# Kernel tuning notes

Measured on AMD Instinct MI355X. Metric: run time of the kernel, lower is better.

## Reference

```python
import jax, jax.numpy as jnp
import numpy as np

STRIDE = 16
SIZES = np.array([128.0, 256.0, 512.0], np.float32)
RATIOS = np.array([0.5, 1.0, 2.0], np.float32)
N_POS, N_NEG = 32, 32          # n_sample=64, pos_ratio=0.5
POS_THR, NEG_THR = 0.7, 0.2
W_CONF, W_REG = 1.0, 5.0


def _conv(x, w, b, stride, pad):
    y = jax.lax.conv_general_dilated(x, w, (stride, stride), [(pad, pad), (pad, pad)],
                                     dimension_numbers=('NCHW', 'OIHW', 'NCHW'))
    return y + b[None, :, None, None]


def _anchors(fw, fh, stride):
    # 9 anchors per center: 3 sizes x 3 aspect ratios
    ws = (SIZES[:, None] * np.sqrt(RATIOS)[None, :]).reshape(-1)
    hs = (SIZES[:, None] / np.sqrt(RATIOS)[None, :]).reshape(-1)
    wh = jnp.asarray(np.stack([ws, hs], -1))                      # (9,2)
    cx = (jnp.arange(fw, dtype=jnp.float32) + 0.5) * stride
    cy = (jnp.arange(fh, dtype=jnp.float32) + 0.5) * stride
    gx, gy = jnp.meshgrid(cx, cy, indexing='ij')                  # x-major, like the torch list comp
    ctr = jnp.stack([gx, gy], -1)[:, :, None, :]                  # (fw,fh,1,2)
    tl = ctr - wh / 2.0
    xywh = jnp.concatenate([tl, jnp.broadcast_to(wh, tl.shape)], -1)  # (fw,fh,9,4)
    return xywh.reshape(-1, 4)


def _xywh_to_xyxy(b):
    return jnp.concatenate([b[:, :2], b[:, :2] + b[:, 2:]], -1)


def _iou(a, b):  # a [N,4], b [M,4], xyxy
    lt = jnp.maximum(a[:, None, :2], b[None, :, :2])
    rb = jnp.minimum(a[:, None, 2:], b[None, :, 2:])
    inter = jnp.clip(rb - lt, 0.0).prod(-1)
    aa = (a[:, 2] - a[:, 0]) * (a[:, 3] - a[:, 1])
    ab = (b[:, 2] - b[:, 0]) * (b[:, 3] - b[:, 1])
    return inter / (aa[:, None] + ab[None, :] - inter)


def _head_flat(y, per):  # [1, 9*per, H, W] -> [W*H*9, per], matching anchor flatten order
    _, _, H, W = y.shape
    return y[0].reshape(9, per, H, W).transpose(3, 2, 0, 1).reshape(-1, per)


def _apply_offsets(boxes, off):  # decode proposals from xyxy boxes + (dx,dy,dw,dh)
    w = boxes[:, 2] - boxes[:, 0]; h = boxes[:, 3] - boxes[:, 1]
    cx = boxes[:, 0] + 0.5 * w;    cy = boxes[:, 1] + 0.5 * h
    ncx = cx + off[:, 0] * w;      ncy = cy + off[:, 1] * h
    nw = w * jnp.exp(off[:, 2]);   nh = h * jnp.exp(off[:, 3])
    return jnp.stack([ncx - nw / 2, ncy - nh / 2, ncx + nw / 2, ncy + nh / 2], -1)


def _box_offset(anc, gt):
    aw = anc[:, 2] - anc[:, 0]; ah = anc[:, 3] - anc[:, 1]
    acx = anc[:, 0] + 0.5 * aw; acy = anc[:, 1] + 0.5 * ah
    gw = gt[:, 2] - gt[:, 0];   gh = gt[:, 3] - gt[:, 1]
    gcx = gt[:, 0] + 0.5 * gw;  gcy = gt[:, 1] + 0.5 * gh
    return jnp.stack([(gcx - acx) / aw, (gcy - acy) / ah,
                      jnp.log(gw / aw), jnp.log(gh / ah)], -1)


def setup_inputs():
    key = jax.random.key(0)
    ks = jax.random.split(key, 12)
    img_data = jax.random.normal(ks[0], (1, 3, 1600, 1600), jnp.float32)
    x1 = jax.random.uniform(ks[1], (64,), minval=0.0, maxval=1400.0)
    y1 = jax.random.uniform(ks[2], (64,), minval=0.0, maxval=1400.0)
    bw = jax.random.uniform(ks[3], (64,), minval=32.0, maxval=200.0)
    bh = jax.random.uniform(ks[4], (64,), minval=32.0, maxval=200.0)
    gt_boxes = jnp.stack([x1, y1, x1 + bw, y1 + bh], -1)[None]   # [1,64,4], all valid (no -1 pad)
    gt_classes = jax.random.randint(ks[5], (1, 64), 1, 21, jnp.int32)
    def w(k, shape, fan):
        return jax.random.normal(k, shape, jnp.float32) * np.float32(np.sqrt(2.0 / fan))
    return dict(
        img_data=img_data, gt_boxes=gt_boxes, gt_classes=gt_classes,
        w1=w(ks[6], (64, 3, 7, 7), 3 * 49),      b1=jnp.zeros(64, jnp.float32),
        w2=w(ks[7], (256, 64, 3, 3), 64 * 9),    b2=jnp.zeros(256, jnp.float32),
        w_rpn=w(ks[8], (256, 256, 3, 3), 256 * 9), b_rpn=jnp.zeros(256, jnp.float32),
        w_cls=w(ks[9], (18, 256, 1, 1), 256),    b_cls=jnp.zeros(18, jnp.float32),
        w_reg=w(ks[10], (36, 256, 1, 1), 256),   b_reg=jnp.zeros(36, jnp.float32),
    )


def reference(img_data, gt_boxes, gt_classes, w1, b1, w2, b2, w_rpn, b_rpn, w_cls, b_cls, w_reg, b_reg):
    # --- feature extractor (total stride 16) ---
    fm = jax.nn.relu(_conv(img_data, w1, b1, 4, 3))
    fm = jax.nn.relu(_conv(fm, w2, b2, 4, 1))            # [1,256,100,100]
    H, W = fm.shape[2], fm.shape[3]
    # --- anchors + IoU matching ---
    anchors_xywh = _anchors(W, H, STRIDE)                # [N,4] xywh
    anchors_xyxy = _xywh_to_xyxy(anchors_xywh)
    gt = gt_boxes[0]                                     # [M,4], all valid
    ious = _iou(anchors_xyxy, gt)                        # [N,M]
    N = ious.shape[0]
    gt_max = ious.max(0)                                 # best iou per gt
    is_gt_best = (ious == gt_max[None, :]).any(1)        # torch: where(iou == gt_max)[0]
    anc_argmax = ious.argmax(1)
    anc_max = ious.max(1)
    labels = jnp.full((N,), -1.0, jnp.float32)
    labels = jnp.where(anc_max < NEG_THR, 0.0, labels)
    labels = jnp.where(is_gt_best, 1.0, labels)
    labels = jnp.where(anc_max > POS_THR, 1.0, labels)
    # --- deterministic pos/neg sampling (fixed sizes; replaces randperm subsampling) ---
    idx = jnp.arange(N, dtype=jnp.float32)
    _, pos_index = jax.lax.top_k(jnp.where(labels == 1.0, anc_max, -1.0), N_POS)
    _, neg_index = jax.lax.top_k(jnp.where(labels == 0.0, 1e6 - idx, -1e9), N_NEG)
    bboxes_pos = anchors_xyxy[pos_index]                 # box_convert(xywh->xyxy) of pos anchors
    # --- proposal module (RPN head) ---
    h = jax.nn.relu(_conv(fm, w_rpn, b_rpn, 1, 1))
    cls = _head_flat(_conv(h, w_cls, b_cls, 1, 0), 2)    # [N,2]
    reg = _head_flat(_conv(h, w_reg, b_reg, 1, 0), 4)    # [N,4]
    pos_score = cls[pos_index]
    neg_score = cls[neg_index]
    offset_pos = reg[pos_index]
    proposals = _apply_offsets(bboxes_pos, offset_pos)
    # --- losses ---
    gt_offset = _box_offset(bboxes_pos, gt[anc_argmax[pos_index]])
    logits = jnp.concatenate([pos_score, neg_score], 0)  # [64,2]
    tgt = jnp.concatenate([jnp.ones(N_POS, jnp.int32), jnp.zeros(N_NEG, jnp.int32)])
    logp = jax.nn.log_softmax(logits, -1)
    cls_loss = -logp[jnp.arange(N_POS + N_NEG), tgt].mean()
    d = gt_offset - offset_pos
    ad = jnp.abs(d)
    reg_loss = jnp.where(ad < 1.0, 0.5 * d * d, ad - 0.5).mean()
    total_rpn_loss = W_CONF * cls_loss + W_REG * reg_loss
    gt_cls_pos = gt_classes[0][anc_argmax[pos_index]]
    return (total_rpn_loss, fm, proposals, pos_index, gt_cls_pos)
```

## Files before the change

### kernel.cpp

```cpp
#include <hip/hip_runtime.h>
#include <math.h>


#define CAP 4096

typedef __attribute__((ext_vector_type(8))) short bf16x8;
typedef __attribute__((ext_vector_type(4))) float f32x4;

__device__ __forceinline__ void dma16(const void* g, void* l) {
    __builtin_amdgcn_global_load_lds((const __attribute__((address_space(1))) void*)g,
                                     (__attribute__((address_space(3))) void*)l, 16, 0, 0);
}

#define OFF_F1T     0
#define OFF_FMT     5171328
#define OFF_CPART   6503040
#define OFF_RPART   7223040
#define OFF_WA1     8663040
#define OFF_W9_2    8672448
#define OFF_W9_3    8746176
#define OFF_WTC     9041088
#define OFF_WTG     9045696
#define OFF_AARG    9054912
#define OFF_NEGM    9144912
#define OFF_POSM    9147728
#define OFF_GTMAX   9150544
#define OFF_CANDS   9150688
#define OFF_CANDI   9154784
#define OFF_IMGB    9158880

__device__ __forceinline__ unsigned short f2bf(float f) {
    unsigned int u = __float_as_uint(f);
    u += 0x7fffu + ((u >> 16) & 1u);
    return (unsigned short)(u >> 16);
}

__device__ __forceinline__ void anchor_box(int i, float& x0, float& y0,
                                           float& x1, float& y1, float& area) {
#pragma clang fp contract(off)
    const float sizes[3]  = {128.f, 256.f, 512.f};
    const float ratios[3] = {0.5f, 1.f, 2.f};
    int a = i % 9;
    int q = i / 9;
    int iy = q % 100;
    int ix = q / 100;
    int s = a / 3, r = a % 3;
    float sq = sqrtf(ratios[r]);
    float w = sizes[s] * sq;
    float h = sizes[s] / sq;
    float cx = ((float)ix + 0.5f) * 16.0f;
    float cy = ((float)iy + 0.5f) * 16.0f;
    x0 = cx - w * 0.5f;
    y0 = cy - h * 0.5f;
    x1 = x0 + w;
    y1 = y0 + h;
    area = (x1 - x0) * (y1 - y0);
}

__device__ __forceinline__ float iou_one(float ax0, float ay0, float ax1, float ay1, float aa,
                                         float bx0, float by0, float bx1, float by1, float ab) {
#pragma clang fp contract(off)
    float ltx = fmaxf(ax0, bx0), lty = fmaxf(ay0, by0);
    float rbx = fminf(ax1, bx1), rby = fminf(ay1, by1);
    float iw = fmaxf(rbx - ltx, 0.0f);
    float ih = fmaxf(rby - lty, 0.0f);
    float inter = iw * ih;
    return inter / ((aa + ab) - inter);
}

__global__ __launch_bounds__(256) void setup_kernel(const float* __restrict__ wc, float* __restrict__ wtc,
                                                    const float* __restrict__ wg, float* __restrict__ wtg,
                                                    const float* __restrict__ w1, unsigned short* __restrict__ wa1,
                                                    const float* __restrict__ w2, unsigned short* __restrict__ w9_2,
                                                    const float* __restrict__ wr, unsigned short* __restrict__ w9_3,
                                                    unsigned int* __restrict__ f1t_u, unsigned int* __restrict__ fmt_u,
                                                    unsigned int* __restrict__ gtmax,
                                                    const float* __restrict__ img, unsigned short* __restrict__ imgb) {
    int i = blockIdx.x * 256 + threadIdx.x;
    if (i < 65) { gtmax[i] = 0u; return; }
    i -= 65;
    if (i < 103040) {
        if (i < 51328) {
            int p = i >> 5, part = i & 31;
            int x, y;
            if (p < 804) { y = (p < 402) ? 0 : 401; x = p % 402; }
            else { int j = p - 804; x = (j < 400) ? 0 : 401; y = 1 + (j % 400); }
            f1t_u[(y * 402 + x) * 32 + part] = 0u;
        } else {
            int i2 = i - 51328;
            int p = i2 >> 7, part = i2 & 127;
            int x, y;
            if (p < 204) { y = (p < 102) ? 0 : 101; x = p % 102; }
            else { int j = p - 204; x = (j < 100) ? 0 : 101; y = 1 + (j % 100); }
            fmt_u[(y * 102 + x) * 128 + part] = 0u;
        }
        return;
    }
    i -= 103040;
    if (i < 4608) { int c = i / 256, k = i - c * 256; wtc[k * 18 + c] = wc[i]; return; }
    i -= 4608;
    if (i < 9216) { int c = i / 256, k = i - c * 256; wtg[k * 36 + c] = wg[i]; return; }
    i -= 9216;
    if (i < 12288) {
        int oc = i / 192, k = i - oc * 192;
        int q = k >> 3, kx = k & 7;
        int ky = q / 3, ic = q - (q / 3) * 3;
        wa1[i] = (q < 21 && kx < 7) ? f2bf(w1[oc * 147 + ic * 49 + ky * 7 + kx])
                                    : (unsigned short)0;
        return;
    }
    i -= 12288;
    if (i < 147456) {
        int cc = i >> 14;
        int rem = i & 16383;
        int ocT = rem >> 10;
        int rem2 = rem & 1023;
        int kcl = rem2 >> 9;
        int lane = (rem2 & 511) >> 3;
        int e = rem2 & 7;
        int oc = ocT * 16 + (lane & 15);
        int ic = kcl * 32 + (lane >> 4) * 8 + e;
        w9_2[i] = f2bf(w2[(oc * 64 + ic) * 9 + cc]);
        return;
    }
    i -= 147456;
    if (i < 589824) {
        int cc = i >> 14;
        int rem = i & 16383;
        int ocT = rem >> 10;
        int rem2 = rem & 1023;
        int kcl = rem2 >> 9;
        int lane = (rem2 & 511) >> 3;
        int e = rem2 & 7;
        int kk = cc >> 2, chv = cc & 3;
        int oc = ocT * 16 + (lane & 15);
        int icl = kcl * 32 + (lane >> 4) * 8 + e;
        w9_3[i] = f2bf(wr[(oc * 256 + chv * 64 + icl) * 9 + kk]);
        return;
    }
    i -= 589824;
    if (i < 7680000) {
        int ic = i / 2560000;
        int rem = i - ic * 2560000;
        int y = rem / 1600, x = rem - (rem / 1600) * 1600;
        imgb[((size_t)(ic * 1608 + y + 3)) * 1608 + x + 3] = f2bf(img[((size_t)(ic * 1600 + y)) * 1600 + x]);
        return;
    }
    i -= 7680000;
    if (i < 38592) {
        int ic = i / 12864;
        int rem = i - ic * 12864;
        int r8 = rem / 1608, xp = rem - r8 * 1608;
        int yp = (r8 < 3) ? r8 : (1600 + r8);
        imgb[((size_t)(ic * 1608 + yp)) * 1608 + xp] = 0;
        return;
    }
    i -= 38592;
    if (i < 28800) {
        int ic = i / 9600;
        int rem = i - ic * 9600;
        int y = rem / 6, xi = rem - (rem / 6) * 6;
        int xp = (xi < 3) ? xi : (1602 + xi);
        imgb[((size_t)(ic * 1608 + y + 3)) * 1608 + xp] = 0;
    }
}

__device__ __forceinline__ void iou1_body(int bid, int t, const float* __restrict__ gt,
                                          int* __restrict__ aarg, unsigned int* __restrict__ gtmax) {
    __shared__ float sg1[64][4];
    __shared__ float sarea1[64];
    __shared__ unsigned int smax1[64];
    if (t < 64) {
#pragma clang fp contract(off)
        float b0 = gt[t * 4 + 0], b1 = gt[t * 4 + 1];
        float b2 = gt[t * 4 + 2], b3 = gt[t * 4 + 3];
        sg1[t][0] = b0; sg1[t][1] = b1; sg1[t][2] = b2; sg1[t][3] = b3;
        sarea1[t] = (b2 - b0) * (b3 - b1);
        smax1[t] = 0u;
    }
    __syncthreads();
    int i = bid * 256 + t;
    int iq = min(i, 89999);
    float x0, y0, x1, y1, aa;
    anchor_box(iq, x0, y0, x1, y1, aa);
    float best = -1.f;
    int bestj = 0;
    for (int j = 0; j < 64; j++) {
        float v = iou_one(x0, y0, x1, y1, aa, sg1[j][0], sg1[j][1], sg1[j][2], sg1[j][3], sarea1[j]);
        if (v > best) { best = v; bestj = j; }
        float vm = v;
#pragma unroll
        for (int off = 32; off > 0; off >>= 1) vm = fmaxf(vm, __shfl_xor(vm, off));
        if ((t & 63) == 0) atomicMax(&smax1[j], __float_as_uint(vm));
    }
    if (i < 90000) aarg[i] = bestj;
    __syncthreads();
    if (t < 64) atomicMax(&gtmax[t], smax1[t]);
}

__device__ __forceinline__ void iou2_body(int bid, int t, const float* __restrict__ gt,
                                          const unsigned int* __restrict__ gtmax,
                                          unsigned long long* __restrict__ negmask,
                                          unsigned long long* __restrict__ posmask,
                                          float* __restrict__ cand_s, int* __restrict__ cand_i,
                                          unsigned int* __restrict__ cnt) {
    __shared__ float sg2[64][4];
    __shared__ float sarea2[64];
    __shared__ float sgm2[64];
    if (t < 64) {
#pragma clang fp contract(off)
        float b0 = gt[t * 4 + 0], b1 = gt[t * 4 + 1];
        float b2 = gt[t * 4 + 2], b3 = gt[t * 4 + 3];
        sg2[t][0] = b0; sg2[t][1] = b1; sg2[t][2] = b2; sg2[t][3] = b3;
        sarea2[t] = (b2 - b0) * (b3 - b1);
        sgm2[t] = __uint_as_float(gtmax[t]);
    }
    __syncthreads();
    int i = bid * 512 + t;
    if (i >= 90000) return;
    float x0, y0, x1, y1, aa;
    anchor_box(i, x0, y0, x1, y1, aa);
    float best = -1.f;
    bool isbest = false;
    for (int j = 0; j < 64; j++) {
        float v = iou_one(x0, y0, x1, y1, aa, sg2[j][0], sg2[j][1], sg2[j][2], sg2[j][3], sarea2[j]);
        if (v > best) best = v;
        if (v == sgm2[j]) isbest = true;
    }
    float label = -1.f;
    if (best < 0.2f) label = 0.f;
    if (isbest) label = 1.f;
    if (best > 0.7f) label = 1.f;
    unsigned long long negb = __ballot(label == 0.f);
    unsigned long long posb = __ballot(label == 1.f);
    if ((t & 63) == 0) { negmask[i >> 6] = negb; posmask[i >> 6] = posb; }
    if (label == 1.f) {
        unsigned int p = atomicAdd(cnt, 1u);
        if (p < CAP) { cand_s[p] = best; cand_i[p] = i; }
    }
}

__device__ __forceinline__ void conv1_body(int bx, int oy, int t,
                                           const unsigned short* __restrict__ imgb,
                                           const unsigned short* __restrict__ wA,
                                           const float* __restrict__ bias,
                                           unsigned short* __restrict__ f1t) {
    __shared__ __align__(16) unsigned char smem[13312];
    unsigned short* win = (unsigned short*)smem;
    unsigned short* tileT = (unsigned short*)smem;
    int wave = t >> 6, lane = t & 63;
    int quad = lane >> 4, l16 = lane & 15;
    int ox0 = bx * 64;
    int col0 = ox0 * 4;
    int gy0 = 4 * oy - 3;
    const size_t ZROW = ((size_t)(2 * 1608 + 1606)) * 1608;

    for (int o = wave; o < 13; o += 4) {
        int q = o * 64 + lane;
        int r = q / 33;
        int c = q - r * 33;
        int rc = min(r, 20);
        int ky = rc / 3, ic = rc - (rc / 3) * 3;
        int yp = gy0 + ky + 3;
        size_t offm = ((size_t)(ic * 1608 + yp)) * 1608 + col0 + c * 8;
        size_t offz = ZROW + (size_t)(q - 693) * 8;
        dma16(imgb + ((r < 21) ? offm : offz), (char*)smem + o * 1024);
    }
    bf16x8 afr[6];
    {
        const bf16x8* ap = (const bf16x8*)(wA + (wave * 16 + l16) * 192 + quad * 8);
#pragma unroll
        for (int c = 0; c < 6; c++) afr[c] = ap[c * 4];
    }
    __syncthreads();

    f32x4 acc[4];
#pragma unroll
    for (int j = 0; j < 4; j++) acc[j] = (f32x4){0.f, 0.f, 0.f, 0.f};
#pragma unroll
    for (int ch = 0; ch < 6; ch++) {
        const unsigned short* wrow = win + (ch * 4 + quad) * 264;
#pragma unroll
        for (int j = 0; j < 4; j++) {
            int px = j * 16 + l16;
            const unsigned long long* bp = (const unsigned long long*)(wrow + 4 * px);
            union { unsigned long long u[2]; bf16x8 v; } uu;
            uu.u[0] = bp[0];
            uu.u[1] = bp[1];
            acc[j] = __builtin_amdgcn_mfma_f32_16x16x32_bf16(afr[ch], uu.v, acc[j], 0, 0, 0);
        }
    }
    __syncthreads();
#pragma unroll
    for (int reg = 0; reg < 4; reg++) {
        int oc = wave * 16 + quad * 4 + reg;
        float bv = bias[oc];
#pragma unroll
        for (int j = 0; j < 4; j++) {
            int px = j * 16 + l16;
            tileT[px * 72 + oc] = f2bf(fmaxf(acc[j][reg] + bv, 0.f));
        }
    }
    __syncthreads();
    int px = t >> 2, part = t & 3;
    int ox = ox0 + px;
    if (ox < 400) {
        int row = (oy + 1) * 402 + ox + 1;
        uint4 v0 = *(const uint4*)(tileT + px * 72 + part * 16);
        uint4 v1 = *(const uint4*)(tileT + px * 72 + part * 16 + 8);
        *(uint4*)(f1t + row * 64 + part * 16) = v0;
        *(uint4*)(f1t + row * 64 + part * 16 + 8) = v1;
    }
}

__global__ __launch_bounds__(256, 4) void conv1_iou1(const unsigned short* __restrict__ imgb,
                                                     const unsigned short* __restrict__ wA,
                                                     const float* __restrict__ bias,
                                                     unsigned short* __restrict__ f1t,
                                                     const float* __restrict__ gt,
                                                     int* __restrict__ aarg,
                                                     unsigned int* __restrict__ gtmax) {
    int t = threadIdx.x;
    if (blockIdx.x < 7) {
        conv1_body(blockIdx.x, blockIdx.y, t, imgb, wA, bias, f1t);
    } else {
        int bid = blockIdx.y;
        if (bid < 352) iou1_body(bid, t, gt, aarg, gtmax);
    }
}

template<int ICC, int RS, int S, bool WRT, bool HEAD>
__device__ __forceinline__ void conv_body(int xs, int y, int t,
                                          const unsigned short* __restrict__ Bt,
                                          const unsigned short* __restrict__ A9,
                                          const float* __restrict__ bias,
                                          float* __restrict__ outF,
                                          unsigned short* __restrict__ outT,
                                          const float* __restrict__ wtc,
                                          const float* __restrict__ wtg,
                                          float* __restrict__ cpart,
                                          float* __restrict__ rpart) {
    constexpr int NC = ICC / 64;
    constexpr int PXB = 13;
    constexpr int HC = S * (PXB - 1) + 3;
    constexpr int CHW = ICC / 8;
    constexpr int TOT = 3 * HC * CHW;
    constexpr int OPS = (TOT + 63) / 64;
    constexpr int BB = OPS * 1024;
    constexpr int SMB = HEAD ? (16384 + 256 * 14 * 4) : BB;
    __shared__ __align__(16) unsigned char smem[SMB < BB ? BB : SMB];
    unsigned short* blds = (unsigned short*)smem;
    float* sred = (float*)smem;
    float* hlds = (float*)(smem + 16384);

    int wave = t >> 6, lane = t & 63;
    int PX = min(PXB, 100 - xs * PXB);

    for (int o = wave; o < OPS; o += 8) {
        int q = min(o * 64 + lane, TOT - 1);
        int row = q / CHW;
        int e = q - row * CHW;
        int ky = row / HC;
        int c = row - ky * HC;
        int s = (S == 4) ? (e ^ ((c >> 2) & 7)) : (e ^ (row & 7));
        const unsigned short* src = Bt + ((size_t)(S * y + ky) * RS + S * xs * PXB + c) * ICC + s * 8;
        dma16(src, (char*)smem + o * 1024);
    }

    int ow = wave & 3, kg = wave >> 2;
    int quad = lane >> 4, l16 = lane & 15;
    int oc0 = ow * 64;
    int pxe = min(l16, PX - 1);
    int swp = pxe & 7;

    f32x4 acc[4];
#pragma unroll
    for (int mt = 0; mt < 4; mt++) acc[mt] = (f32x4){0.f, 0.f, 0.f, 0.f};

    const bf16x8* Av = (const bf16x8*)A9;
    __syncthreads();

    constexpr int NS = (NC == 1) ? 9 : 36;
    bf16x8 afA[4], afB[4];
    {
        int cc0 = (NC == 1) ? 0 : kg * 18;
        int kl0 = (NC == 1) ? kg : 0;
#pragma unroll
        for (int mt = 0; mt < 4; mt++)
            afA[mt] = Av[(size_t)cc0 * 2048 + (ow * 4 + mt) * 128 + kl0 * 64 + lane];
    }
    auto kstep = [&](int s, bf16x8 (&cur)[4], bf16x8 (&nxt)[4]) {
        int cc  = (NC == 1) ? s : kg * 18 + (s >> 1);
        int kcl = (NC == 1) ? kg : (s & 1);
        int pass = cc / NC, ch = cc - pass * NC;
        int ky = pass / 3, kx = pass - (pass / 3) * 3;
        int row = ky * HC + S * pxe + kx;
        int ck = kcl * 4 + quad;
        int chunk = (S == 4) ? (ck ^ swp) : ((ch * 8 + ck) ^ (row & 7));
        bf16x8 bf = *(const bf16x8*)(blds + row * ICC + chunk * 8);
        if (s + 1 < NS) {
            int cn = (NC == 1) ? (s + 1) : kg * 18 + ((s + 1) >> 1);
            int kn = (NC == 1) ? kg : ((s + 1) & 1);
#pragma unroll
            for (int mt = 0; mt < 4; mt++)
                nxt[mt] = Av[(size_t)cn * 2048 + (ow * 4 + mt) * 128 + kn * 64 + lane];
        }
#pragma unroll
        for (int mt = 0; mt < 4; mt++)
            acc[mt] = __builtin_amdgcn_mfma_f32_16x16x32_bf16(cur[mt], bf, acc[mt], 0, 0, 0);
    };
#pragma unroll
    for (int s2 = 0; s2 < NS; s2 += 2) {
        kstep(s2, afA, afB);
        if (s2 + 1 < NS) kstep(s2 + 1, afB, afA);
    }

    __syncthreads();
    if (kg == 1) {
#pragma unroll
        for (int mt = 0; mt < 4; mt++)
            *(f32x4*)(sred + ((ow * 4 + mt) * 64 + lane) * 4) = acc[mt];
    }
    __syncthreads();
    if (kg == 0) {
#pragma unroll
        for (int mt = 0; mt < 4; mt++) {
            f32x4 o = *(const f32x4*)(sred + ((ow * 4 + mt) * 64 + lane) * 4);
            acc[mt] = acc[mt] + o;
        }
#pragma unroll
        for (int mt = 0; mt < 4; mt++) {
#pragma unroll
            for (int reg = 0; reg < 4; reg++) {
                int oc = oc0 + mt * 16 + quad * 4 + reg;
                float bv = bias[oc];
                int pl = l16;
                if (pl < PX) {
                    float v = fmaxf(acc[mt][reg] + bv, 0.f);
                    if (HEAD) {
                        hlds[oc * 14 + pl] = v;
                    } else {
                        int p = y * 100 + xs * PXB + pl;
                        outF[oc * 10000 + p] = v;
                        if (WRT) {
                            int r = (y + 1) * 102 + xs * PXB + pl + 1;
                            outT[r * 256 + oc] = f2bf(v);
                        }
                    }
                }
            }
        }
    }
    if (HEAD) {
        __syncthreads();
        int base = y * 100 + xs * PXB;
        for (int it = t; it < 2808; it += 512) {
            int ch = it / 702;
            int r = it - ch * 702;
            int j = r / 13;
            int p = r - j * 13;
            if (p < PX) {
                int jc = (j < 18) ? j : (j - 18);
                const float* wt = (j < 18) ? (wtc + jc) : (wtg + jc);
                int stride = (j < 18) ? 18 : 36;
                int ic0 = ch * 64;
                float acc2 = 0.f;
#pragma unroll 8
                for (int ic = 0; ic < 64; ic++)
                    acc2 += hlds[(ic0 + ic) * 14 + p] * wt[(ic0 + ic) * stride];
                float* dst = (j < 18) ? (cpart + (ch * 18 + jc) * 10000)
                                      : (rpart + (ch * 36 + jc) * 10000);
                dst[base + p] = acc2;
            }
        }
    }
}

__global__ __launch_bounds__(512, 4) void conv2_iou2(const unsigned short* __restrict__ Bt,
                                                     const unsigned short* __restrict__ A9,
                                                     const float* __restrict__ bias,
                                                     float* __restrict__ outF,
                                                     unsigned short* __restrict__ outT,
                                                     const float* __restrict__ gt,
                                                     const unsigned int* __restrict__ gtmax,
                                                     unsigned long long* __restrict__ negmask,
                                                     unsigned long long* __restrict__ posmask,
                                                     float* __restrict__ cand_s,
                                                     int* __restrict__ cand_i,
                                                     unsigned int* __restrict__ cnt) {
    int t = threadIdx.x;
    if (blockIdx.x < 8) {
        conv_body<64, 402, 4, true, false>(blockIdx.x, blockIdx.y, t, Bt, A9, bias,
                                           outF, outT, nullptr, nullptr, nullptr, nullptr);
    } else {
        int bid = (blockIdx.x - 8) * 100 + blockIdx.y;
        if (bid < 176) iou2_body(bid, t, gt, gtmax, negmask, posmask, cand_s, cand_i, cnt);
    }
}

__global__ __launch_bounds__(512, 4) void conv3_head(const unsigned short* __restrict__ Bt,
                                                     const unsigned short* __restrict__ A9,
                                                     const float* __restrict__ bias,
                                                     const float* __restrict__ wtc,
                                                     const float* __restrict__ wtg,
                                                     float* __restrict__ cpart,
                                                     float* __restrict__ rpart) {
    conv_body<256, 102, 1, false, true>(blockIdx.x, blockIdx.y, threadIdx.x, Bt, A9, bias,
                                        nullptr, nullptr, wtc, wtg, cpart, rpart);
}

__device__ __forceinline__ unsigned long long shflx64(unsigned long long v, int m) {
    int lo = __shfl_xor((int)(unsigned)(v & 0xFFFFFFFFull), m);
    int hi = __shfl_xor((int)(unsigned)(v >> 32), m);
    return ((unsigned long long)(unsigned)hi << 32) | (unsigned)lo;
}

__device__ int wave_first32(const unsigned long long* __restrict__ mask,
                            bool invert, int* __restrict__ outIdx, int lane) {
    const int NW = 1407;
    const int WPT = 22;
    unsigned long long mw[WPT];
    int cnt = 0;
#pragma unroll
    for (int u = 0; u < WPT; u++) {
        int w = lane * WPT + u;
        unsigned long long m = 0ull;
        if (w < NW) {
            m = mask[w];
            if (invert) m = ~m;
            if (w == NW - 1) m &= 0xFFFFull;
        }
        mw[u] = m;
        cnt += __builtin_popcountll(m);
    }
    int inc = cnt;
#pragma unroll
    for (int off = 1; off < 64; off <<= 1) {
        int v = __shfl_up(inc, off);
        if (lane >= off) inc += v;
    }
    int total = __shfl(inc, 63);
    int pref = inc - cnt;
    if (pref < 32) {
#pragma unroll
        for (int u = 0; u < WPT; u++) {
            unsigned long long m = mw[u];
            int wbase = (lane * WPT + u) * 64;
            while (m && pref < 32) {
                int b = __builtin_ctzll(m);
                outIdx[pref++] = wbase + b;
                m &= m - 1;
            }
        }
    }
    return total;
}

__global__ __launch_bounds__(64) void tail_kernel(const unsigned long long* __restrict__ negmask,
                                                  const unsigned long long* __restrict__ posmask,
                                                  const float* __restrict__ cand_s,
                                                  const int* __restrict__ cand_i,
                                                  const unsigned int* __restrict__ cnt,
                                                  const float* __restrict__ cpart,
                                                  const float* __restrict__ rpart,
                                                  const float* __restrict__ bcls,
                                                  const float* __restrict__ breg,
                                                  const int* __restrict__ aarg,
                                                  const float* __restrict__ gt,
                                                  const int* __restrict__ gtc,
                                                  float* __restrict__ out) {
    __shared__ unsigned long long keys[CAP + 32];
    __shared__ int sfill[32];
    __shared__ int spidx[32];
    __shared__ int snidx[32];
    int lane = threadIdx.x;

    int ncand = min((int)*cnt, CAP);
    for (int c = lane; c < ncand; c += 64) {
        unsigned u = __float_as_uint(cand_s[c]);
        u ^= (u & 0x80000000u) ? 0xFFFFFFFFu : 0x80000000u;
        keys[c] = ((unsigned long long)u << 32) | (0xFFFFFFFFu - (unsigned)cand_i[c]);
    }
    int ntot = ncand;
    if (ncand < 32) {
        int tot = wave_first32(posmask, true, sfill, lane);
        int nfill = min(tot, 32);
        unsigned um1 = __float_as_uint(-1.0f) ^ 0xFFFFFFFFu;
        for (int k2 = lane; k2 < nfill; k2 += 64)
            keys[ncand + k2] = ((unsigned long long)um1 << 32) | (0xFFFFFFFFu - (unsigned)sfill[k2]);
        ntot += nfill;
    }

    unsigned long long lk = 0ull; int ls = -1;
    for (int c = lane; c < ntot; c += 64) {
        unsigned long long k = keys[c];
        if (k > lk) { lk = k; ls = c; }
    }
    for (int s = 0; s < 32; s++) {
        unsigned long long mk = lk;
#pragma unroll
        for (int off = 1; off < 64; off <<= 1) {
            unsigned long long o = shflx64(mk, off);
            if (o > mk) mk = o;
        }
        if (lk == mk && mk != 0ull) {
            spidx[s] = (int)(0xFFFFFFFFu - (unsigned)(mk & 0xFFFFFFFFull));
            keys[ls] = 0ull;
            lk = 0ull; ls = -1;
            for (int c = lane; c < ntot; c += 64) {
                unsigned long long k = keys[c];
                if (k > lk) { lk = k; ls = c; }
            }
        }
    }

    int totn = wave_first32(negmask, false, snidx, lane);
    if (lane == 0) {
        int nf = min(totn, 32);
        for (int s = nf; s < 32; s++) snidx[s] = s;
    }

    {
#pragma clang fp contract(off)
        const int PROP_OFF = 1 + 2560000;
        int t = lane;
        int n = (t < 32) ? spidx[t] : snidx[t - 32];
        int a = n % 9;
        int q = n / 9;
        int iy = q % 100;
        int ix = q / 100;
        int p = iy * 100 + ix;

        float l0 = bcls[a * 2 + 0], l1 = bcls[a * 2 + 1];
        for (int c = 0; c < 4; c++) {
            l0 += cpart[(c * 18 + a * 2 + 0) * 10000 + p];
            l1 += cpart[(c * 18 + a * 2 + 1) * 10000 + p];
        }
        float m = fmaxf(l0, l1);
        float lse = m + logf(expf(l0 - m) + expf(l1 - m));
        float logp = ((t < 32) ? l1 : l0) - lse;
        float cls_sum = logp;
#pragma unroll
        for (int off = 32; off > 0; off >>= 1) cls_sum += __shfl_down(cls_sum, off);

        float reg_sum = 0.f;
        if (t < 32) {
            float offv[4];
#pragma unroll
            for (int k = 0; k < 4; k++) {
                float v = breg[a * 4 + k];
                for (int c = 0; c < 4; c++) v += rpart[(c * 36 + a * 4 + k) * 10000 + p];
                offv[k] = v;
            }
            float x0, y0, x1, y1, aa;
            anchor_box(n, x0, y0, x1, y1, aa);
            float w = x1 - x0, h = y1 - y0;
            float cx = x0 + 0.5f * w, cy = y0 + 0.5f * h;
            float ncx = cx + offv[0] * w, ncy = cy + offv[1] * h;
            float nw = w * expf(offv[2]), nh = h * expf(offv[3]);
            out[PROP_OFF + t * 4 + 0] = ncx - nw * 0.5f;
            out[PROP_OFF + t * 4 + 1] = ncy - nh * 0.5f;
            out[PROP_OFF + t * 4 + 2] = ncx + nw * 0.5f;
            out[PROP_OFF + t * 4 + 3] = ncy + nh * 0.5f;

            int j = aarg[n];
            float g0 = gt[j * 4 + 0], g1 = gt[j * 4 + 1];
            float g2 = gt[j * 4 + 2], g3 = gt[j * 4 + 3];
            float gw = g2 - g0, gh = g3 - g1;
            float gcx = g0 + 0.5f * gw, gcy = g1 + 0.5f * gh;
            float tg[4];
            tg[0] = (gcx - cx) / w;
            tg[1] = (gcy - cy) / h;
            tg[2] = logf(gw / w);
            tg[3] = logf(gh / h);
#pragma unroll
            for (int k = 0; k < 4; k++) {
                float d = tg[k] - offv[k];
                float ad = fabsf(d);
                reg_sum += (ad < 1.f) ? 0.5f * d * d : ad - 0.5f;
            }
            out[PROP_OFF + 128 + t] = (float)n;
            out[PROP_OFF + 160 + t] = (float)gtc[j];
        }
#pragma unroll
        for (int off = 32; off > 0; off >>= 1) reg_sum += __shfl_down(reg_sum, off);
        if (t == 0) {
            float cls_loss = -(cls_sum / 64.f);
            float reg_loss = reg_sum / 128.f;
            out[0] = cls_loss + 5.f * reg_loss;
        }
    }
}

extern "C" void kernel_launch(void* const* d_in, const int* in_sizes, int n_in,
                              void* d_out, int out_size, void* d_ws, size_t ws_size,
                              hipStream_t stream) {
    const float* img = (const float*)d_in[0];
    const float* gt  = (const float*)d_in[1];
    const int*   gtc = (const int*)d_in[2];
    const float* w1  = (const float*)d_in[3];
    const float* b1  = (const float*)d_in[4];
    const float* w2  = (const float*)d_in[5];
    const float* b2  = (const float*)d_in[6];
    const float* wr  = (const float*)d_in[7];
    const float* br  = (const float*)d_in[8];
    const float* wc  = (const float*)d_in[9];
    const float* bc  = (const float*)d_in[10];
    const float* wg  = (const float*)d_in[11];
    const float* bg  = (const float*)d_in[12];
    float* out = (float*)d_out;
    float* ws = (float*)d_ws;

    unsigned short* f1t  = (unsigned short*)(ws + OFF_F1T);
    unsigned short* fmt  = (unsigned short*)(ws + OFF_FMT);
    unsigned short* wa1  = (unsigned short*)(ws + OFF_WA1);
    unsigned short* w9_2 = (unsigned short*)(ws + OFF_W9_2);
    unsigned short* w9_3 = (unsigned short*)(ws + OFF_W9_3);
    unsigned short* imgb = (unsigned short*)(ws + OFF_IMGB);
    float* cpart = ws + OFF_CPART;
    float* rpart = ws + OFF_RPART;
    float* wtc   = ws + OFF_WTC;
    float* wtg   = ws + OFF_WTG;
    int*   aarg  = (int*)(ws + OFF_AARG);
    unsigned long long* negm = (unsigned long long*)(ws + OFF_NEGM);
    unsigned long long* posm = (unsigned long long*)(ws + OFF_POSM);
    unsigned int* gtmax = (unsigned int*)(ws + OFF_GTMAX);
    unsigned int* cnt   = gtmax + 64;
    float* cands = ws + OFF_CANDS;
    int*   candi = (int*)(ws + OFF_CANDI);
    float* fm    = out + 1;

    setup_kernel<<<dim3(33649), dim3(256), 0, stream>>>(wc, wtc, wg, wtg, w1, wa1,
                                                        w2, w9_2, wr, w9_3,
                                                        (unsigned int*)f1t, (unsigned int*)fmt, gtmax,
                                                        img, imgb);

    conv1_iou1<<<dim3(8, 400), dim3(256), 0, stream>>>(imgb, wa1, b1, f1t, gt, aarg, gtmax);
    conv2_iou2<<<dim3(10, 100), dim3(512), 0, stream>>>(f1t, w9_2, b2, fm, fmt,
                                                        gt, gtmax, negm, posm, cands, candi, cnt);
    conv3_head<<<dim3(8, 100), dim3(512), 0, stream>>>(fmt, w9_3, br, wtc, wtg, cpart, rpart);
    tail_kernel<<<dim3(1), dim3(64), 0, stream>>>(negm, posm, cands, candi, cnt,
                                                  cpart, rpart, bc, bg, aarg, gt, gtc, out);
}
```

Baseline: 296.5 us.

## Widen conv tiles to 25 pixels and stage weights through double-buffered LDS

Each conv block now covers 25 output pixels per row, with the 8 waves split into two 16-pixel halves instead of two K-groups. That removes the cross-wave reduction through shared memory. Weight tiles are re-laid out per (cc,kcl) unit and streamed into a double-buffered LDS region with async global-to-LDS loads, replacing per-lane global register loads. Grids shrink to 4 column-blocks per row. The trade-offs are a __syncthreads per K-step, larger LDS use, and 7 of 32 pixel lanes per block wasted, while activation halo reloads are amortised over more pixels.

```diff
diff --git a/kernel.cpp b/kernel.cpp
--- a/kernel.cpp
+++ b/kernel.cpp
@@ -111,13 +111,13 @@
     }
     i -= 12288;
     if (i < 147456) {
-        int cc = i >> 14;
-        int rem = i & 16383;
-        int ocT = rem >> 10;
-        int rem2 = rem & 1023;
-        int kcl = rem2 >> 9;
-        int lane = (rem2 & 511) >> 3;
+        int unit = i >> 13;
+        int rem = i & 8191;
+        int ocT = rem >> 9;
+        int rem2 = rem & 511;
+        int lane = rem2 >> 3;
         int e = rem2 & 7;
+        int cc = unit >> 1, kcl = unit & 1;
         int oc = ocT * 16 + (lane & 15);
         int ic = kcl * 32 + (lane >> 4) * 8 + e;
         w9_2[i] = f2bf(w2[(oc * 64 + ic) * 9 + cc]);
@@ -125,13 +125,13 @@
     }
     i -= 147456;
     if (i < 589824) {
-        int cc = i >> 14;
-        int rem = i & 16383;
-        int ocT = rem >> 10;
-        int rem2 = rem & 1023;
-        int kcl = rem2 >> 9;
-        int lane = (rem2 & 511) >> 3;
+        int unit = i >> 13;
+        int rem = i & 8191;
+        int ocT = rem >> 9;
+        int rem2 = rem & 511;
+        int lane = rem2 >> 3;
         int e = rem2 & 7;
+        int cc = unit >> 1, kcl = unit & 1;
         int kk = cc >> 2, chv = cc & 3;
         int oc = ocT * 16 + (lane & 15);
         int icl = kcl * 32 + (lane >> 4) * 8 + e;
@@ -341,111 +341,81 @@
                                           float* __restrict__ cpart,
                                           float* __restrict__ rpart) {
     constexpr int NC = ICC / 64;
-    constexpr int PXB = 13;
-    constexpr int HC = S * (PXB - 1) + 3;
+    constexpr int HC = S * 24 + 3;
     constexpr int CHW = ICC / 8;
     constexpr int TOT = 3 * HC * CHW;
-    constexpr int OPS = (TOT + 63) / 64;
-    constexpr int BB = OPS * 1024;
-    constexpr int SMB = HEAD ? (16384 + 256 * 14 * 4) : BB;
-    __shared__ __align__(16) unsigned char smem[SMB < BB ? BB : SMB];
+    constexpr int BOPS = (TOT + 63) / 64;
+    constexpr int BB = BOPS * 1024;
+    constexpr int NS = (NC == 1) ? 18 : 72;
+    __shared__ __align__(16) unsigned char smem[BB + 32768];
     unsigned short* blds = (unsigned short*)smem;
-    float* sred = (float*)smem;
-    float* hlds = (float*)(smem + 16384);
+    float* hlds = (float*)(smem + BB);
 
     int wave = t >> 6, lane = t & 63;
-    int PX = min(PXB, 100 - xs * PXB);
-
-    for (int o = wave; o < OPS; o += 8) {
+    int ow = wave & 3, ph = wave >> 2;
+    int quad = lane >> 4, l16 = lane & 15;
+    int oc0 = ow * 64;
+    int pl = ph * 16 + l16;
+    int pxe = min(pl, 24);
+    int swp = pxe & 7;
+
+    for (int o = wave; o < BOPS; o += 8) {
         int q = min(o * 64 + lane, TOT - 1);
         int row = q / CHW;
         int e = q - row * CHW;
         int ky = row / HC;
         int c = row - ky * HC;
-        int s = (S == 4) ? (e ^ ((c >> 2) & 7)) : (e ^ (row & 7));
-        const unsigned short* src = Bt + ((size_t)(S * y + ky) * RS + S * xs * PXB + c) * ICC + s * 8;
-        dma16(src, (char*)smem + o * 1024);
-    }
-
-    int ow = wave & 3, kg = wave >> 2;
-    int quad = lane >> 4, l16 = lane & 15;
-    int oc0 = ow * 64;
-    int pxe = min(l16, PX - 1);
-    int swp = pxe & 7;
+        int sz = (S == 4) ? (e ^ ((c >> 2) & 7)) : (e ^ (row & 7));
+        dma16(Bt + ((size_t)(S * y + ky) * RS + S * xs * 25 + c) * ICC + sz * 8,
+              (char*)smem + o * 1024);
+    }
+    for (int o = wave; o < 16; o += 8)
+        dma16(A9 + (size_t)(o * 64 + lane) * 8, (char*)smem + BB + o * 1024);
 
     f32x4 acc[4];
 #pragma unroll
     for (int mt = 0; mt < 4; mt++) acc[mt] = (f32x4){0.f, 0.f, 0.f, 0.f};
-
-    const bf16x8* Av = (const bf16x8*)A9;
     __syncthreads();
 
-    constexpr int NS = (NC == 1) ? 9 : 36;
-    bf16x8 afA[4], afB[4];
-    {
-        int cc0 = (NC == 1) ? 0 : kg * 18;
-        int kl0 = (NC == 1) ? kg : 0;
-#pragma unroll
-        for (int mt = 0; mt < 4; mt++)
-            afA[mt] = Av[(size_t)cc0 * 2048 + (ow * 4 + mt) * 128 + kl0 * 64 + lane];
-    }
-    auto kstep = [&](int s, bf16x8 (&cur)[4], bf16x8 (&nxt)[4]) {
-        int cc  = (NC == 1) ? s : kg * 18 + (s >> 1);
-        int kcl = (NC == 1) ? kg : (s & 1);
+    for (int u = 0; u < NS; u++) {
+        if (u + 1 < NS) {
+            char* dst = (char*)smem + BB + ((u + 1) & 1) * 16384;
+            const unsigned short* src = A9 + (size_t)(u + 1) * 8192;
+            for (int o = wave; o < 16; o += 8)
+                dma16(src + (size_t)(o * 64 + lane) * 8, dst + o * 1024);
+        }
+        const unsigned short* ab = (const unsigned short*)(smem + BB + (u & 1) * 16384);
+        int cc = u >> 1, kcl = u & 1;
         int pass = cc / NC, ch = cc - pass * NC;
         int ky = pass / 3, kx = pass - (pass / 3) * 3;
         int row = ky * HC + S * pxe + kx;
         int ck = kcl * 4 + quad;
         int chunk = (S == 4) ? (ck ^ swp) : ((ch * 8 + ck) ^ (row & 7));
         bf16x8 bf = *(const bf16x8*)(blds + row * ICC + chunk * 8);
-        if (s + 1 < NS) {
-            int cn = (NC == 1) ? (s + 1) : kg * 18 + ((s + 1) >> 1);
-            int kn = (NC == 1) ? kg : ((s + 1) & 1);
-#pragma unroll
-            for (int mt = 0; mt < 4; mt++)
-                nxt[mt] = Av[(size_t)cn * 2048 + (ow * 4 + mt) * 128 + kn * 64 + lane];
-        }
-#pragma unroll
-        for (int mt = 0; mt < 4; mt++)
-            acc[mt] = __builtin_amdgcn_mfma_f32_16x16x32_bf16(cur[mt], bf, acc[mt], 0, 0, 0);
-    };
-#pragma unroll
-    for (int s2 = 0; s2 < NS; s2 += 2) {
-        kstep(s2, afA, afB);
-        if (s2 + 1 < NS) kstep(s2 + 1, afB, afA);
-    }
-
-    __syncthreads();
-    if (kg == 1) {
-#pragma unroll
-        for (int mt = 0; mt < 4; mt++)
-            *(f32x4*)(sred + ((ow * 4 + mt) * 64 + lane) * 4) = acc[mt];
-    }
-    __syncthreads();
-    if (kg == 0) {
 #pragma unroll
         for (int mt = 0; mt < 4; mt++) {
-            f32x4 o = *(const f32x4*)(sred + ((ow * 4 + mt) * 64 + lane) * 4);
-            acc[mt] = acc[mt] + o;
-        }
-#pragma unroll
-        for (int mt = 0; mt < 4; mt++) {
-#pragma unroll
-            for (int reg = 0; reg < 4; reg++) {
-                int oc = oc0 + mt * 16 + quad * 4 + reg;
-                float bv = bias[oc];
-                int pl = l16;
-                if (pl < PX) {
-                    float v = fmaxf(acc[mt][reg] + bv, 0.f);
-                    if (HEAD) {
-                        hlds[oc * 14 + pl] = v;
-                    } else {
-                        int p = y * 100 + xs * PXB + pl;
-                        outF[oc * 10000 + p] = v;
-                        if (WRT) {
-                            int r = (y + 1) * 102 + xs * PXB + pl + 1;
-                            outT[r * 256 + oc] = f2bf(v);
-                        }
+            bf16x8 af = *(const bf16x8*)(ab + ((ow * 4 + mt) * 64 + lane) * 8);
+            acc[mt] = __builtin_amdgcn_mfma_f32_16x16x32_bf16(af, bf, acc[mt], 0, 0, 0);
+        }
+        __syncthreads();
+    }
+
+#pragma unroll
+    for (int mt = 0; mt < 4; mt++) {
+#pragma unroll
+        for (int reg = 0; reg < 4; reg++) {
+            int oc = oc0 + mt * 16 + quad * 4 + reg;
+            float bv = bias[oc];
+            if (pl < 25) {
+                float v = fmaxf(acc[mt][reg] + bv, 0.f);
+                if (HEAD) {
+                    hlds[oc * 26 + pl] = v;
+                } else {
+                    int p = y * 100 + xs * 25 + pl;
+                    outF[oc * 10000 + p] = v;
+                    if (WRT) {
+                        int r = (y + 1) * 102 + xs * 25 + pl + 1;
+                        outT[r * 256 + oc] = f2bf(v);
                     }
                 }
             }
@@ -453,25 +423,23 @@
     }
     if (HEAD) {
         __syncthreads();
-        int base = y * 100 + xs * PXB;
-        for (int it = t; it < 2808; it += 512) {
-            int ch = it / 702;
-            int r = it - ch * 702;
-            int j = r / 13;
-            int p = r - j * 13;
-            if (p < PX) {
-                int jc = (j < 18) ? j : (j - 18);
-                const float* wt = (j < 18) ? (wtc + jc) : (wtg + jc);
-                int stride = (j < 18) ? 18 : 36;
-                int ic0 = ch * 64;
-                float acc2 = 0.f;
+        int base = y * 100 + xs * 25;
+        for (int it = t; it < 5400; it += 512) {
+            int ch = it / 1350;
+            int r = it - ch * 1350;
+            int j = r / 25;
+            int p = r - j * 25;
+            int jc = (j < 18) ? j : (j - 18);
+            const float* wt = (j < 18) ? (wtc + jc) : (wtg + jc);
+            int stride = (j < 18) ? 18 : 36;
+            int ic0 = ch * 64;
+            float acc2 = 0.f;
 #pragma unroll 8
-                for (int ic = 0; ic < 64; ic++)
-                    acc2 += hlds[(ic0 + ic) * 14 + p] * wt[(ic0 + ic) * stride];
-                float* dst = (j < 18) ? (cpart + (ch * 18 + jc) * 10000)
-                                      : (rpart + (ch * 36 + jc) * 10000);
-                dst[base + p] = acc2;
-            }
+            for (int ic = 0; ic < 64; ic++)
+                acc2 += hlds[(ic0 + ic) * 26 + p] * wt[(ic0 + ic) * stride];
+            float* dst = (j < 18) ? (cpart + (ch * 18 + jc) * 10000)
+                                  : (rpart + (ch * 36 + jc) * 10000);
+            dst[base + p] = acc2;
         }
     }
 }
@@ -489,11 +457,11 @@
                                                      int* __restrict__ cand_i,
                                                      unsigned int* __restrict__ cnt) {
     int t = threadIdx.x;
-    if (blockIdx.x < 8) {
+    if (blockIdx.x < 4) {
         conv_body<64, 402, 4, true, false>(blockIdx.x, blockIdx.y, t, Bt, A9, bias,
                                            outF, outT, nullptr, nullptr, nullptr, nullptr);
     } else {
-        int bid = (blockIdx.x - 8) * 100 + blockIdx.y;
+        int bid = (blockIdx.x - 4) * 100 + blockIdx.y;
         if (bid < 176) iou2_body(bid, t, gt, gtmax, negmask, posmask, cand_s, cand_i, cnt);
     }
 }
@@ -736,9 +704,9 @@
                                                         img, imgb);
 
     conv1_iou1<<<dim3(8, 400), dim3(256), 0, stream>>>(imgb, wa1, b1, f1t, gt, aarg, gtmax);
-    conv2_iou2<<<dim3(10, 100), dim3(512), 0, stream>>>(f1t, w9_2, b2, fm, fmt,
-                                                        gt, gtmax, negm, posm, cands, candi, cnt);
-    conv3_head<<<dim3(8, 100), dim3(512), 0, stream>>>(fmt, w9_3, br, wtc, wtg, cpart, rpart);
+    conv2_iou2<<<dim3(6, 100), dim3(512), 0, stream>>>(f1t, w9_2, b2, fm, fmt,
+                                                       gt, gtmax, negm, posm, cands, candi, cnt);
+    conv3_head<<<dim3(4, 100), dim3(512), 0, stream>>>(fmt, w9_3, br, wtc, wtg, cpart, rpart);
     tail_kernel<<<dim3(1), dim3(64), 0, stream>>>(negm, posm, cands, candi, cnt,
                                                   cpart, rpart, bc, bg, aarg, gt, gtc, out);
 }
```

Result: slower. 303.1 us (+2.2%).
